# Kernel optimization log

Hardware: AMD Instinct MI355X
Metric: run time of the kernel (lower is better)

Reference implementation:

```python
import jax, jax.numpy as jnp
import numpy as np

LOCAL_REGION = 16
GRANULARITY = 2048
INIT_RATIO = 8
EXPAND_RATIO = 2
C = 128
N_LAYERS = 5


def setup_inputs() -> dict:
    key = jax.random.key(0)
    ks = jax.random.split(key, 20)
    g = lambda k, s: jax.random.normal(k, s, dtype=jnp.float32) * 0.05
    z = lambda n: jnp.zeros((n,), jnp.float32)
    return {
        "batch_x": jax.random.normal(ks[0], (1, 16384, 4), dtype=jnp.float32),
        # PT: attr embedding (in_channel=1 -> 128), positional MLP (3->128->128)
        "attr_w": g(ks[1], (1, C)), "attr_b": z(C),
        "pos_w1": g(ks[2], (3, C)), "pos_b1": z(C),
        "pos_w2": g(ks[3], (C, C)), "pos_b2": z(C),
        # 5 self-attention layers over the K-neighborhood
        "wq": g(ks[4], (N_LAYERS, C, C)),
        "wk": g(ks[5], (N_LAYERS, C, C)),
        "wv": g(ks[6], (N_LAYERS, C, C)),
        "wout": g(ks[7], (C, C)), "bout": z(C),
        # mu/sigma head: 128 -> 64 -> 16 -> 2
        "ms_w1": g(ks[8], (C, 64)), "ms_b1": z(64),
        "ms_w2": g(ks[9], (64, 16)), "ms_b2": z(16),
        "ms_w3": g(ks[10], (16, 2)), "ms_b3": z(2),
    }


def _window_schedule(N):
    base = min(N // INIT_RATIO, GRANULARITY)
    win = base
    sched = []
    cursor = base
    while cursor < N:
        win = min(win * EXPAND_RATIO, GRANULARITY)
        sched.append((cursor, min(win, N - cursor)))
        cursor += win
    return sched


def _forward(batch_x, attr_w, attr_b, pos_w1, pos_b1, pos_w2, pos_b2,
             wq, wk, wv, wout, bout, ms_w1, ms_b1, ms_w2, ms_b2, ms_w3, ms_b3):
    B, N, _ = batch_x.shape
    total_bits = jnp.float32(0.0)
    for cur, w in _window_schedule(N):
        context = batch_x[:, :cur, :]
        target = batch_x[:, cur:cur + w, :]
        tg, ta = target[..., :3], target[..., 3:]    # [B,M,3], [B,M,1]
        cg, ca = context[..., :3], context[..., 3:]  # [B,Nc,3], [B,Nc,1]
        # knn_points: brute-force squared distances, K smallest
        d2 = (jnp.sum(tg * tg, -1)[:, :, None] + jnp.sum(cg * cg, -1)[:, None, :]
              - 2.0 * jnp.einsum('bmd,bnd->bmn', tg, cg))  # [B,M,Nc]
        _, idx = jax.lax.top_k(-d2, LOCAL_REGION)            # [B,M,K]
        # knn_gather
        gg = jnp.take_along_axis(cg[:, None], idx[..., None], axis=2)  # [B,M,K,3]
        ga = jnp.take_along_axis(ca[:, None], idx[..., None], axis=2)  # [B,M,K,1]
        # n_scale_ball: center each neighborhood, scale into unit ball
        gg = gg - jnp.mean(gg, axis=2, keepdims=True)
        r = jnp.max(jnp.linalg.norm(gg, axis=-1, keepdims=True), axis=2, keepdims=True)
        gg = gg / jnp.maximum(r, 1e-8)
        # PT: pos-encoded grouped self-attention, max-pool over K
        pos = jax.nn.relu(gg @ pos_w1 + pos_b1) @ pos_w2 + pos_b2  # [B,M,K,C]
        f = ga @ attr_w + attr_b + pos
        for l in range(N_LAYERS):
            q, k, v = f @ wq[l], f @ wk[l], f @ wv[l]
            a = jax.nn.softmax(jnp.einsum('bmkc,bmjc->bmkj', q, k)
                               / jnp.sqrt(jnp.float32(C)), axis=-1)
            f = f + jnp.einsum('bmkj,bmjc->bmkc', a, v)
        feat = jnp.max(f @ wout + bout, axis=2)  # [B,M,C]
        # mu/sigma head
        h = jax.nn.relu(feat @ ms_w1 + ms_b1)
        h = jax.nn.relu(h @ ms_w2 + ms_b2)
        ms = h @ ms_w3 + ms_b3
        mu, sigma = ms[..., :1], jnp.exp(ms[..., 1:])
        # feature_probs_based_mu_sigma: bits under quantized Gaussian
        inv = 1.0 / (sigma * jnp.sqrt(jnp.float32(2.0)))
        probs = 0.5 * (jax.lax.erf((ta + 0.5 - mu) * inv)
                       - jax.lax.erf((ta - 0.5 - mu) * inv))
        total_bits = total_bits + jnp.sum(jnp.clip(-jnp.log2(probs + 1e-10), 0.0, 50.0))
    return total_bits


def reference(batch_x, attr_w, attr_b, pos_w1, pos_b1, pos_w2, pos_b2,
              wq, wk, wv, wout, bout, ms_w1, ms_b1, ms_w2, ms_b2, ms_w3, ms_b3):
    return _forward(batch_x, attr_w, attr_b, pos_w1, pos_b1, pos_w2, pos_b2,
                    wq, wk, wv, wout, bout, ms_w1, ms_b1, ms_w2, ms_b2, ms_w3, ms_b3)
```

## Files before the change

### kernel.cpp

```cpp
#include <hip/hip_runtime.h>
#include <math.h>

#define NPTS 16384
#define WWIN 2048
#define NWIN 7
#define KNB  16
#define CDIM 128
#define NTGT (NPTS - WWIN)
#define TPB  4
#define NBLK (NTGT / TPB)
#define NMAT 12

typedef _Float16 f16;
typedef __attribute__((ext_vector_type(8))) _Float16 f16x8;
typedef __attribute__((ext_vector_type(4))) _Float16 f16x4;
typedef __attribute__((ext_vector_type(2))) _Float16 f16x2;
typedef __attribute__((ext_vector_type(4))) float f32x4;

#define MFMA16(a, b, c) __builtin_amdgcn_mfma_f32_16x16x32_f16((a), (b), (c), 0, 0, 0)

__device__ __forceinline__ unsigned umax_(unsigned a, unsigned b) { return a > b ? a : b; }
__device__ __forceinline__ unsigned umin_(unsigned a, unsigned b) { return a < b ? a : b; }

__global__ void prep_kernel(const float* __restrict__ pos_w2,
                            const float* __restrict__ wq,
                            const float* __restrict__ wk,
                            const float* __restrict__ wv,
                            const float* __restrict__ wout,
                            f16* __restrict__ wt) {
  const int i = blockIdx.x * 256 + threadIdx.x;
  if (i >= NMAT * 16384) return;
  const int mat = i >> 14;
  const int e   = i & 16383;
  const int k   = e >> 7;
  const int n   = e & 127;
  if (mat < 7) {
    const float* src = (mat == 0) ? pos_w2 : (mat <= 5 ? wv + (mat - 1) * 16384 : wout);
    wt[mat * 16384 + n * 128 + k] = (f16)src[k * 128 + n];
  } else {
    const int l = mat - 7;
    const float* qr = wq + l * 16384 + k * 128;
    const float* kr = wk + l * 16384 + n * 128;
    float sacc = 0.f;
#pragma unroll 4
    for (int c = 0; c < 128; ++c) sacc += qr[c] * kr[c];
    wt[mat * 16384 + n * 128 + k] = (f16)sacc;
  }
}

__device__ __forceinline__ f16x8 ldA(const f16* __restrict__ buf, int l15, int lg,
                                     int mt, int kc) {
  const int row = mt * 16 + l15;
  const int col = (kc * 32 + lg * 8) ^ ((row & 7) << 3);
  return *(const f16x8*)(buf + row * 128 + col);
}

__device__ __forceinline__ void stD(f16* __restrict__ buf, int l15, int lg, int n0,
                                    int mt, int nt, const f32x4 v) {
#pragma unroll
  for (int r = 0; r < 4; ++r) {
    const int row = mt * 16 + lg * 4 + r;
    const int col = (n0 + nt * 16 + l15) ^ ((row & 7) << 3);
    buf[row * 128 + col] = (f16)v[r];
  }
}

__device__ __forceinline__ void zacc(f32x4 (&acc)[4][2]) {
#pragma unroll
  for (int mt = 0; mt < 4; ++mt)
#pragma unroll
    for (int nt = 0; nt < 2; ++nt) acc[mt][nt] = (f32x4){0.f, 0.f, 0.f, 0.f};
}

__device__ __forceinline__ void gemm_tile(const f16* __restrict__ src,
                                          const f16* __restrict__ wmat,
                                          int l15, int lg, int n0,
                                          f32x4 (&acc)[4][2]) {
  f16x8 b[4][2];
#pragma unroll
  for (int kc = 0; kc < 4; ++kc) {
    b[kc][0] = *(const f16x8*)(wmat + (n0 + l15) * 128 + kc * 32 + lg * 8);
    b[kc][1] = *(const f16x8*)(wmat + (n0 + 16 + l15) * 128 + kc * 32 + lg * 8);
  }
#pragma unroll
  for (int kc = 0; kc < 4; ++kc) {
#pragma unroll
    for (int mt = 0; mt < 4; ++mt) {
      const f16x8 a = ldA(src, l15, lg, mt, kc);
      acc[mt][0] = MFMA16(a, b[kc][0], acc[mt][0]);
      acc[mt][1] = MFMA16(a, b[kc][1], acc[mt][1]);
    }
  }
}

__global__ __launch_bounds__(256, 2)
void nn_kernel(
    const float4* __restrict__ bx, const f16* __restrict__ wt,
    const float* __restrict__ attr_w, const float* __restrict__ attr_b,
    const float* __restrict__ pos_w1, const float* __restrict__ pos_b1,
    const float* __restrict__ pos_b2, const float* __restrict__ bout,
    const float* __restrict__ ms_w1, const float* __restrict__ ms_b1,
    const float* __restrict__ ms_w2, const float* __restrict__ ms_b2,
    const float* __restrict__ ms_w3, const float* __restrict__ ms_b3,
    float* __restrict__ partials) {
  __shared__ __align__(16) f16 fA[64 * 128];
  __shared__ __align__(16) f16 qA[64 * 128];
  __shared__ __align__(16) f16 pA[TPB * 512];

  const int t     = threadIdx.x;
  const int wv    = t >> 6;
  const int lane  = t & 63;
  const int l15   = lane & 15;
  const int lg    = lane >> 4;
  const int n0    = wv * 32;
  const int slot0 = (NBLK - 1 - blockIdx.x) * TPB;

  {
    const int  slot = slot0 + wv;
    const int  cur  = WWIN * ((slot0 >> 11) + 1);
    const float4 tp = bx[WWIN + slot];

    unsigned u0 = 0xFFFFFFF0u, u1 = 0xFFFFFFF1u, u2 = 0xFFFFFFF2u, u3 = 0xFFFFFFF3u;

#define INS4(P) { const unsigned p_ = (P);                                     \
    const unsigned t0 = umax_(u0, p_); u0 = umin_(u0, p_);                     \
    const unsigned t1 = umax_(u1, t0); u1 = umin_(u1, t0);                     \
    const unsigned t2 = umax_(u2, t1); u2 = umin_(u2, t1);                     \
    u3 = umin_(u3, t2); }

    float4 ca = bx[lane];
    float4 cb = bx[lane + 64];
    for (int j = lane; j < cur; j += 128) {
      const float4 na = bx[j + 128];
      const float4 nb = bx[j + 192];
      const float dx0 = tp.x - ca.x, dy0 = tp.y - ca.y, dz0 = tp.z - ca.z;
      const float dx1 = tp.x - cb.x, dy1 = tp.y - cb.y, dz1 = tp.z - cb.z;
      const float d20 = dx0 * dx0 + dy0 * dy0 + dz0 * dz0;
      const float d21 = dx1 * dx1 + dy1 * dy1 + dz1 * dz1;
      const unsigned p0 = ((__float_as_uint(d20) << 1) & 0xFFFFC000u) | (unsigned)j;
      const unsigned p1 = ((__float_as_uint(d21) << 1) & 0xFFFFC000u) | (unsigned)(j + 64);
      INS4(p0)
      INS4(p1)
      ca = na; cb = nb;
    }
#undef INS4

    unsigned* nbr = ((unsigned*)pA) + 960;
    for (int n = 0; n < 16; ++n) {
      unsigned m = u0;
      m = umin_(m, (unsigned)__shfl_xor((int)m, 1));
      m = umin_(m, (unsigned)__shfl_xor((int)m, 2));
      m = umin_(m, (unsigned)__shfl_xor((int)m, 4));
      m = umin_(m, (unsigned)__shfl_xor((int)m, 8));
      m = umin_(m, (unsigned)__shfl_xor((int)m, 16));
      m = umin_(m, (unsigned)__shfl_xor((int)m, 32));
      if (lane == n) nbr[wv * 16 + n] = m & 0x3FFFu;
      if (u0 == m) {
        u0 = u1; u1 = u2; u2 = u3; u3 = 0xFFFFFFFFu;
      }
    }
  }
  __syncthreads();

  float* ggs = (float*)pA;
  if (t < 64) {
    const int nid  = (int)(((unsigned*)pA)[960 + t]);
    const float4 p = bx[nid];
    float sx = p.x, sy = p.y, sz = p.z;
#pragma unroll
    for (int m = 1; m < 16; m <<= 1) {
      sx += __shfl_xor(sx, m); sy += __shfl_xor(sy, m); sz += __shfl_xor(sz, m);
    }
    const float gx = p.x - sx * 0.0625f;
    const float gy = p.y - sy * 0.0625f;
    const float gz = p.z - sz * 0.0625f;
    float nr = sqrtf(gx * gx + gy * gy + gz * gz);
#pragma unroll
    for (int m = 1; m < 16; m <<= 1) nr = fmaxf(nr, __shfl_xor(nr, m));
    const float inv = 1.f / fmaxf(nr, 1e-8f);
    ggs[t * 4 + 0] = gx * inv; ggs[t * 4 + 1] = gy * inv;
    ggs[t * 4 + 2] = gz * inv; ggs[t * 4 + 3] = p.w;
  }
  __syncthreads();

  {
    const int row = t & 63;
    const int cb  = (t >> 6) * 32;
    const float gx = ggs[row * 4], gy = ggs[row * 4 + 1], gz = ggs[row * 4 + 2];
#pragma unroll
    for (int c = cb; c < cb + 32; c += 2) {
      const float h0 = pos_b1[c]     + gx * pos_w1[c]     + gy * pos_w1[128 + c]     + gz * pos_w1[256 + c];
      const float h1 = pos_b1[c + 1] + gx * pos_w1[c + 1] + gy * pos_w1[128 + c + 1] + gz * pos_w1[256 + c + 1];
      f16x2 pr; pr[0] = (f16)fmaxf(h0, 0.f); pr[1] = (f16)fmaxf(h1, 0.f);
      *(f16x2*)(qA + row * 128 + (c ^ ((row & 7) << 3))) = pr;
    }
  }
  __syncthreads();

  {
    f32x4 acc[4][2];
    zacc(acc);
    gemm_tile(qA, wt, l15, lg, n0, acc);
#pragma unroll
    for (int nt = 0; nt < 2; ++nt) {
      const int col = n0 + nt * 16 + l15;
      const float bias = pos_b2[col] + attr_b[col];
      const float aw   = attr_w[col];
#pragma unroll
      for (int mt = 0; mt < 4; ++mt) {
        f32x4 v = acc[mt][nt];
#pragma unroll
        for (int r = 0; r < 4; ++r)
          v[r] += bias + ggs[(mt * 16 + lg * 4 + r) * 4 + 3] * aw;
        stD(fA, l15, lg, n0, mt, nt, v);
      }
    }
  }
  __syncthreads();

  *(f16x8*)(pA + t * 8) = (f16x8){0, 0, 0, 0, 0, 0, 0, 0};

  for (int l = 0; l < 5; ++l) {
    {
      f32x4 acc[4][2];
      zacc(acc);
      gemm_tile(fA, wt + (7 + l) * 16384, l15, lg, n0, acc);
#pragma unroll
      for (int mt = 0; mt < 4; ++mt)
#pragma unroll
        for (int nt = 0; nt < 2; ++nt) stD(qA, l15, lg, n0, mt, nt, acc[mt][nt]);
    }
    __syncthreads();
    {
      f32x4 s = (f32x4){0.f, 0.f, 0.f, 0.f};
#pragma unroll
      for (int kc = 0; kc < 4; ++kc)
        s = MFMA16(ldA(qA, l15, lg, wv, kc), ldA(fA, l15, lg, wv, kc), s);
#pragma unroll
      for (int r = 0; r < 4; ++r) {
        float v = s[r] * 0.08838834764831844055f;
        float mx = v;
#pragma unroll
        for (int m = 1; m < 16; m <<= 1) mx = fmaxf(mx, __shfl_xor(mx, m));
        const float e = __expf(v - mx);
        float sm = e;
#pragma unroll
        for (int m = 1; m < 16; m <<= 1) sm += __shfl_xor(sm, m);
        pA[wv * 512 + (lg * 4 + r) * 32 + l15] = (f16)(e / sm);
      }
    }
    __syncthreads();
    f16* vt = qA;
    {
      f32x4 acc[4][2];
      zacc(acc);
      gemm_tile(fA, wt + (1 + l) * 16384, l15, lg, n0, acc);
#pragma unroll
      for (int mt = 0; mt < 4; ++mt)
#pragma unroll
        for (int nt = 0; nt < 2; ++nt) {
          const int ch = n0 + nt * 16 + l15;
          const int r0 = (mt * 16 + lg * 4) ^ ((ch & 7) << 3);
          f16x4 p;
#pragma unroll
          for (int r = 0; r < 4; ++r) p[r] = (f16)acc[mt][nt][r];
          *(f16x4*)(vt + ch * 64 + r0) = p;
        }
    }
    __syncthreads();
    {
#pragma unroll
      for (int tt = 0; tt < 4; ++tt) {
        const f16x8 a = *(const f16x8*)(pA + tt * 512 + l15 * 32 + lg * 8);
#pragma unroll
        for (int nt = 0; nt < 2; ++nt) {
          const int colb = n0 + nt * 16 + l15;
          f32x4 c;
#pragma unroll
          for (int r = 0; r < 4; ++r) {
            const int row = tt * 16 + lg * 4 + r;
            c[r] = (float)fA[row * 128 + (colb ^ ((row & 7) << 3))];
          }
          const int r0 = (tt * 16 + 8 * (lg & 1)) ^ ((colb & 7) << 3);
          const f16x8 b = *(const f16x8*)(vt + colb * 64 + r0);
          c = MFMA16(a, b, c);
          stD(fA, l15, lg, n0, tt, nt, c);
        }
      }
    }
    __syncthreads();
  }

  float* feats = (float*)pA;
  float* h1s   = feats + 512;
  float* h2s   = h1s + 256;
  float* btmp  = h2s + 64;
  {
    f32x4 acc[4][2];
    zacc(acc);
    gemm_tile(fA, wt + 6 * 16384, l15, lg, n0, acc);
#pragma unroll
    for (int nt = 0; nt < 2; ++nt) {
      const int col = n0 + nt * 16 + l15;
      const float bo = bout[col];
#pragma unroll
      for (int mt = 0; mt < 4; ++mt) {
        const f32x4 v = acc[mt][nt];
        float m = fmaxf(fmaxf(v[0], v[1]), fmaxf(v[2], v[3])) + bo;
        m = fmaxf(m, __shfl_xor(m, 16));
        m = fmaxf(m, __shfl_xor(m, 32));
        if (lg == 0) feats[mt * 128 + col] = m;
      }
    }
  }
  __syncthreads();
  {
    const int tt = t >> 6, h = t & 63;
    float a = ms_b1[h];
#pragma unroll 4
    for (int c = 0; c < 128; ++c) a += feats[tt * 128 + c] * ms_w1[c * 64 + h];
    h1s[tt * 64 + h] = fmaxf(a, 0.f);
  }
  __syncthreads();
  if (t < 64) {
    const int tt = t >> 4, h = t & 15;
    float a = ms_b2[h];
#pragma unroll 4
    for (int c = 0; c < 64; ++c) a += h1s[tt * 64 + c] * ms_w2[c * 16 + h];
    h2s[tt * 16 + h] = fmaxf(a, 0.f);
  }
  __syncthreads();
  if (t < TPB) {
    float mu = ms_b3[0], lgs = ms_b3[1];
#pragma unroll
    for (int c = 0; c < 16; ++c) {
      mu  += h2s[t * 16 + c] * ms_w3[2 * c];
      lgs += h2s[t * 16 + c] * ms_w3[2 * c + 1];
    }
    const float sigma = expf(lgs);
    const float inv   = 1.f / (sigma * 1.41421356237309504880f);
    const float ta    = ((const float*)bx)[(WWIN + slot0 + t) * 4 + 3];
    const float p = 0.5f * (erff((ta + 0.5f - mu) * inv) - erff((ta - 0.5f - mu) * inv));
    float bits = -log2f(p + 1e-10f);
    btmp[t] = fminf(fmaxf(bits, 0.f), 50.f);
  }
  __syncthreads();
  if (t == 0) partials[blockIdx.x] = btmp[0] + btmp[1] + btmp[2] + btmp[3];
}

__global__ void reduce_kernel(const float* __restrict__ partials, float* __restrict__ out) {
  float s = 0.f;
  for (int i = threadIdx.x; i < NBLK; i += 256) s += partials[i];
#pragma unroll
  for (int m = 1; m < 64; m <<= 1) s += __shfl_xor(s, m);
  __shared__ float wsum[4];
  if ((threadIdx.x & 63) == 0) wsum[threadIdx.x >> 6] = s;
  __syncthreads();
  if (threadIdx.x == 0) out[0] = wsum[0] + wsum[1] + wsum[2] + wsum[3];
}

extern "C" void kernel_launch(void* const* d_in, const int* in_sizes, int n_in,
                              void* d_out, int out_size, void* d_ws, size_t ws_size,
                              hipStream_t stream) {
  const float4* bx     = (const float4*)d_in[0];
  const float* attr_w  = (const float*)d_in[1];
  const float* attr_b  = (const float*)d_in[2];
  const float* pos_w1  = (const float*)d_in[3];
  const float* pos_b1  = (const float*)d_in[4];
  const float* pos_w2  = (const float*)d_in[5];
  const float* pos_b2  = (const float*)d_in[6];
  const float* wq      = (const float*)d_in[7];
  const float* wk      = (const float*)d_in[8];
  const float* wv      = (const float*)d_in[9];
  const float* wout    = (const float*)d_in[10];
  const float* bout    = (const float*)d_in[11];
  const float* ms_w1   = (const float*)d_in[12];
  const float* ms_b1   = (const float*)d_in[13];
  const float* ms_w2   = (const float*)d_in[14];
  const float* ms_b2   = (const float*)d_in[15];
  const float* ms_w3   = (const float*)d_in[16];
  const float* ms_b3   = (const float*)d_in[17];

  f16*   wt       = (f16*)((char*)d_ws);
  float* partials = (float*)((char*)d_ws + (1u << 19));

  prep_kernel<<<(NMAT * 16384 + 255) / 256, 256, 0, stream>>>(pos_w2, wq, wk, wv, wout, wt);
  nn_kernel<<<NBLK, 256, 0, stream>>>(bx, wt, attr_w, attr_b,
                                      pos_w1, pos_b1, pos_b2, bout,
                                      ms_w1, ms_b1, ms_w2, ms_b2, ms_w3, ms_b3,
                                      partials);
  reduce_kernel<<<1, 256, 0, stream>>>(partials, (float*)d_out);
}
```

Measured before the change: 402.7 us.

## Keep residual features in registers and merge Q/V GEMM phases to cut barriers

Adds a separate LDS buffer for the transposed V tile so the Q and V projections can both run before a single barrier, dropping one __syncthreads per layer. The residual feature state is now kept in fp32 MFMA accumulators across layers instead of being re-read from fp16 LDS before each residual add, which removes those LDS reads and an fp16 round-trip on the residual. The weight-fragment loads in the GEMM tile are moved inside the k loop to lower register pressure. In exchange, LDS use grows by 16KB per block and register pressure rises from holding the persistent accumulators, which may affect occupancy under launch_bounds(256,2).

```diff
diff --git a/kernel.cpp b/kernel.cpp
--- a/kernel.cpp
+++ b/kernel.cpp
@@ -76,19 +76,15 @@
                                           const f16* __restrict__ wmat,
                                           int l15, int lg, int n0,
                                           f32x4 (&acc)[4][2]) {
-  f16x8 b[4][2];
 #pragma unroll
   for (int kc = 0; kc < 4; ++kc) {
-    b[kc][0] = *(const f16x8*)(wmat + (n0 + l15) * 128 + kc * 32 + lg * 8);
-    b[kc][1] = *(const f16x8*)(wmat + (n0 + 16 + l15) * 128 + kc * 32 + lg * 8);
-  }
-#pragma unroll
-  for (int kc = 0; kc < 4; ++kc) {
+    const f16x8 b0 = *(const f16x8*)(wmat + (n0 + l15) * 128 + kc * 32 + lg * 8);
+    const f16x8 b1 = *(const f16x8*)(wmat + (n0 + 16 + l15) * 128 + kc * 32 + lg * 8);
 #pragma unroll
     for (int mt = 0; mt < 4; ++mt) {
       const f16x8 a = ldA(src, l15, lg, mt, kc);
-      acc[mt][0] = MFMA16(a, b[kc][0], acc[mt][0]);
-      acc[mt][1] = MFMA16(a, b[kc][1], acc[mt][1]);
+      acc[mt][0] = MFMA16(a, b0, acc[mt][0]);
+      acc[mt][1] = MFMA16(a, b1, acc[mt][1]);
     }
   }
 }
@@ -105,6 +101,7 @@
     float* __restrict__ partials) {
   __shared__ __align__(16) f16 fA[64 * 128];
   __shared__ __align__(16) f16 qA[64 * 128];
+  __shared__ __align__(16) f16 vtB[128 * 64];
   __shared__ __align__(16) f16 pA[TPB * 512];
 
   const int t     = threadIdx.x;
@@ -197,10 +194,10 @@
   }
   __syncthreads();
 
-  {
-    f32x4 acc[4][2];
-    zacc(acc);
-    gemm_tile(qA, wt, l15, lg, n0, acc);
+  f32x4 facc[4][2];
+  {
+    zacc(facc);
+    gemm_tile(qA, wt, l15, lg, n0, facc);
 #pragma unroll
     for (int nt = 0; nt < 2; ++nt) {
       const int col = n0 + nt * 16 + l15;
@@ -208,11 +205,10 @@
       const float aw   = attr_w[col];
 #pragma unroll
       for (int mt = 0; mt < 4; ++mt) {
-        f32x4 v = acc[mt][nt];
 #pragma unroll
         for (int r = 0; r < 4; ++r)
-          v[r] += bias + ggs[(mt * 16 + lg * 4 + r) * 4 + 3] * aw;
-        stD(fA, l15, lg, n0, mt, nt, v);
+          facc[mt][nt][r] += bias + ggs[(mt * 16 + lg * 4 + r) * 4 + 3] * aw;
+        stD(fA, l15, lg, n0, mt, nt, facc[mt][nt]);
       }
     }
   }
@@ -229,30 +225,6 @@
       for (int mt = 0; mt < 4; ++mt)
 #pragma unroll
         for (int nt = 0; nt < 2; ++nt) stD(qA, l15, lg, n0, mt, nt, acc[mt][nt]);
-    }
-    __syncthreads();
-    {
-      f32x4 s = (f32x4){0.f, 0.f, 0.f, 0.f};
-#pragma unroll
-      for (int kc = 0; kc < 4; ++kc)
-        s = MFMA16(ldA(qA, l15, lg, wv, kc), ldA(fA, l15, lg, wv, kc), s);
-#pragma unroll
-      for (int r = 0; r < 4; ++r) {
-        float v = s[r] * 0.08838834764831844055f;
-        float mx = v;
-#pragma unroll
-        for (int m = 1; m < 16; m <<= 1) mx = fmaxf(mx, __shfl_xor(mx, m));
-        const float e = __expf(v - mx);
-        float sm = e;
-#pragma unroll
-        for (int m = 1; m < 16; m <<= 1) sm += __shfl_xor(sm, m);
-        pA[wv * 512 + (lg * 4 + r) * 32 + l15] = (f16)(e / sm);
-      }
-    }
-    __syncthreads();
-    f16* vt = qA;
-    {
-      f32x4 acc[4][2];
       zacc(acc);
       gemm_tile(fA, wt + (1 + l) * 16384, l15, lg, n0, acc);
 #pragma unroll
@@ -264,27 +236,40 @@
           f16x4 p;
 #pragma unroll
           for (int r = 0; r < 4; ++r) p[r] = (f16)acc[mt][nt][r];
-          *(f16x4*)(vt + ch * 64 + r0) = p;
+          *(f16x4*)(vtB + ch * 64 + r0) = p;
         }
     }
     __syncthreads();
     {
+      f32x4 s = (f32x4){0.f, 0.f, 0.f, 0.f};
+#pragma unroll
+      for (int kc = 0; kc < 4; ++kc)
+        s = MFMA16(ldA(qA, l15, lg, wv, kc), ldA(fA, l15, lg, wv, kc), s);
+#pragma unroll
+      for (int r = 0; r < 4; ++r) {
+        float v = s[r] * 0.08838834764831844055f;
+        float mx = v;
+#pragma unroll
+        for (int m = 1; m < 16; m <<= 1) mx = fmaxf(mx, __shfl_xor(mx, m));
+        const float e = __expf(v - mx);
+        float sm = e;
+#pragma unroll
+        for (int m = 1; m < 16; m <<= 1) sm += __shfl_xor(sm, m);
+        pA[wv * 512 + (lg * 4 + r) * 32 + l15] = (f16)(e / sm);
+      }
+    }
+    __syncthreads();
+    {
 #pragma unroll
       for (int tt = 0; tt < 4; ++tt) {
         const f16x8 a = *(const f16x8*)(pA + tt * 512 + l15 * 32 + lg * 8);
 #pragma unroll
         for (int nt = 0; nt < 2; ++nt) {
           const int colb = n0 + nt * 16 + l15;
-          f32x4 c;
-#pragma unroll
-          for (int r = 0; r < 4; ++r) {
-            const int row = tt * 16 + lg * 4 + r;
-            c[r] = (float)fA[row * 128 + (colb ^ ((row & 7) << 3))];
-          }
           const int r0 = (tt * 16 + 8 * (lg & 1)) ^ ((colb & 7) << 3);
-          const f16x8 b = *(const f16x8*)(vt + colb * 64 + r0);
-          c = MFMA16(a, b, c);
-          stD(fA, l15, lg, n0, tt, nt, c);
+          const f16x8 b = *(const f16x8*)(vtB + colb * 64 + r0);
+          facc[tt][nt] = MFMA16(a, b, facc[tt][nt]);
+          stD(fA, l15, lg, n0, tt, nt, facc[tt][nt]);
         }
       }
     }
```

New measurement: 386.6 us. -4.0%, faster.
